# Kernel optimization log

Hardware: AMD Instinct MI355X
Metric: run time of the kernel (lower is better)

## Reference

```python
import jax, jax.numpy as jnp
import numpy as np

EPS = 1e-12  # matches torch F.normalize default eps
SCALE = 64.0  # fixed softmax temperature from the source

def _l2_normalize(x, axis):
    n = jnp.linalg.norm(x, ord=2, axis=axis, keepdims=True)
    return x / jnp.maximum(n, EPS)

def setup_inputs() -> dict:
    key = jax.random.key(0)
    k1, k2, k3 = jax.random.split(key, 3)
    B, L, S, D = 8, 2048, 2048, 128
    return {
        "query": jax.random.normal(k1, (B, L, D), dtype=jnp.float32),
        "key": jax.random.normal(k2, (B, S, D), dtype=jnp.float32),
        "value": jax.random.normal(k3, (B, S, D), dtype=jnp.float32),
    }

def reference(query, key, value):
    # rank-3 query path with norm=True, return_value=True, return_score=False
    q = _l2_normalize(query, axis=2)   # [B, L, D]
    k = _l2_normalize(key, axis=2)     # [B, S, D]
    score = jnp.einsum('nlk,nsk->nls', q, k)            # [B, L, S]
    score = jax.nn.softmax(score * SCALE, axis=2)
    # original does broadcast-multiply-then-sum; equivalent contraction:
    out = jnp.einsum('nls,nsd->nld', score, value)      # [B, L, D]
    return out
```

## Files before the change

### kernel.cpp

```cpp
#include <hip/hip_runtime.h>
#include <stdint.h>

#define Bb 8
#define Ll 2048
#define Ss 2048
#define Dd 128
#define NSB 8
#define SCHUNK 256
#define NROWS 16384
#define SCALE_LOG2E 92.33248261689366f

typedef __attribute__((ext_vector_type(8))) short bf16x8;
typedef __attribute__((ext_vector_type(16))) float f32x16;
typedef __attribute__((ext_vector_type(4))) unsigned u32x4;

__device__ __forceinline__ unsigned f2bf_pack(float a, float b) {
  unsigned ua = __float_as_uint(a); ua += 0x7fffu + ((ua >> 16) & 1u);
  unsigned ub = __float_as_uint(b); ub += 0x7fffu + ((ub >> 16) & 1u);
  return (ua >> 16) | (ub & 0xffff0000u);
}

__device__ __forceinline__ unsigned pkbf(float a, float b) {
#if __has_builtin(__builtin_amdgcn_cvt_pk_bf16_f32)
  auto r = __builtin_amdgcn_cvt_pk_bf16_f32(a, b);
  return __builtin_bit_cast(unsigned, r);
#else
  return f2bf_pack(a, b);
#endif
}

__device__ __forceinline__ void gl_lds16(const void* g, void* l) {
  __builtin_amdgcn_global_load_lds(
      (const __attribute__((address_space(1))) unsigned*)g,
      (__attribute__((address_space(3))) unsigned*)l, 16, 0, 0);
}


#define TRS 138
extern "C" __global__ __launch_bounds__(256)
void prep_kern(const float* __restrict__ Q, const float* __restrict__ K,
               const float* __restrict__ V,
               unsigned short* __restrict__ Qn, unsigned short* __restrict__ Kf,
               unsigned short* __restrict__ Vf) {
  __shared__ unsigned short T[32 * TRS];
  const int t = threadIdx.x;
  const int bid = blockIdx.x;
  if (bid < 8192) {
    const int lane = t & 63;
    int row = (bid << 2) + (t >> 6);
    const bool isK = row >= NROWS;
    const int r = isK ? row - NROWS : row;
    const float* src = isK ? K : Q;
    float2 f = *(const float2*)(src + (size_t)r * Dd + lane * 2);
    float ss = f.x * f.x + f.y * f.y;
#pragma unroll
    for (int m = 1; m < 64; m <<= 1) ss += __shfl_xor(ss, m, 64);
    float inv = 1.0f / fmaxf(sqrtf(ss), 1e-12f);
    unsigned w = pkbf(f.x * inv, f.y * inv);
    if (!isK) {
      *(unsigned*)(Qn + (size_t)r * Dd + lane * 2) = w;
    } else {
      const int srow = r & (Ss - 1);
      const int b = r >> 11;
      size_t off = (((size_t)b * 64 + (srow >> 5)) * 8 + (lane >> 3)) * 512 +
                   (((lane >> 2) & 1) * 32 + (srow & 31)) * 8 + ((2 * lane) & 7);
      *(unsigned*)(Kf + off) = w;
    }
  } else {
    const int vb = bid - 8192;
    const int b = vb & 7, sw = vb >> 3;
    const int d4 = t & 31, sr = t >> 5;
#pragma unroll
    for (int p = 0; p < 4; ++p) {
      int sl = p * 8 + sr;
      float4 v = *(const float4*)(V + ((size_t)(b * Ss + sw * 32 + sl)) * Dd + d4 * 4);
      *(unsigned*)&T[sl * TRS + d4 * 4]     = pkbf(v.x, v.y);
      *(unsigned*)&T[sl * TRS + d4 * 4 + 2] = pkbf(v.z, v.w);
    }
    __syncthreads();
    const int so = t & 3, db = t >> 2;
    const int t2 = so >> 1, h = so & 1;
#pragma unroll
    for (int p = 0; p < 2; ++p) {
      int d = p * 64 + db;
      unsigned u[4];
#pragma unroll
      for (int k = 0; k < 4; ++k) {
        unsigned lo = T[(so * 8 + 2 * k) * TRS + d];
        unsigned hi = T[(so * 8 + 2 * k + 1) * TRS + d];
        u[k] = lo | (hi << 16);
      }
      const int vslot = (d >> 5) * 2 + t2;
      size_t off = (((size_t)b * 64 + sw) * 8 + vslot) * 512 +
                   (h * 32 + (d & 31)) * 8;
      *(uint4*)(Vf + off) = make_uint4(u[0], u[1], u[2], u[3]);
    }
  }
}

extern "C" __global__ __launch_bounds__(256, 4)
void attn_kern(const unsigned short* __restrict__ Qn,
               const unsigned short* __restrict__ Kf,
               const unsigned short* __restrict__ Vf,
               unsigned short* __restrict__ Op,
               float* __restrict__ Lp) {
  __shared__ unsigned short Kl[2][8 * 512];
  __shared__ unsigned short Vl[2][8 * 512];
  const int tid = threadIdx.x, wv = tid >> 6, lane = tid & 63;
  const int lm = lane & 31, h = lane >> 5;
  const int gid = blockIdx.x;
  const int qt = gid >> 6, b = (gid >> 3) & 7, sb = gid & 7;
  const int sblk0 = sb * (SCHUNK / 32);
  const int qrow = qt * 128 + wv * 32 + lm;

  const unsigned short* Qrow = Qn + ((size_t)(b * Ll + qrow)) * Dd;
  bf16x8 qf[8];
#pragma unroll
  for (int kt = 0; kt < 8; ++kt)
    qf[kt] = *(const bf16x8*)(Qrow + kt * 16 + h * 8);

  const unsigned short* Kc = Kf + ((size_t)b * 64 + sblk0) * 8 * 512;
  const unsigned short* Vc = Vf + ((size_t)b * 64 + sblk0) * 8 * 512;

  f32x16 o[4];
#pragma unroll
  for (int i = 0; i < 4; ++i)
#pragma unroll
    for (int r = 0; r < 16; ++r) o[i][r] = 0.f;

  auto stage = [&](int it, int buf) {
    const size_t base = (size_t)it * 4096;
#pragma unroll
    for (int i = 0; i < 2; ++i) {
      const int sl = wv * 2 + i;
      gl_lds16(Kc + base + sl * 512 + lane * 8, &Kl[buf][sl * 512]);
      gl_lds16(Vc + base + sl * 512 + lane * 8, &Vl[buf][sl * 512]);
    }
  };
  stage(0, 0);

  float lrun = 0.f;

#pragma unroll 1
  for (int it = 0; it < 8; ++it) {
    __syncthreads();
    const int cur = it & 1;
    if (it + 1 < 8) stage(it + 1, cur ^ 1);

    f32x16 acc;
#pragma unroll
    for (int r = 0; r < 16; ++r) acc[r] = 0.f;
#pragma unroll
    for (int kt = 0; kt < 8; ++kt) {
      bf16x8 kf = *(const bf16x8*)&Kl[cur][kt * 512 + lane * 8];
      acc = __builtin_amdgcn_mfma_f32_32x32x16_bf16(kf, qf[kt], acc, 0, 0, 0);
    }

    float ls = 0.f;
#pragma unroll
    for (int t = 0; t < 2; ++t) {
      float p[8];
#pragma unroll
      for (int j = 0; j < 8; ++j)
        p[j] = __builtin_amdgcn_exp2f(
            __builtin_fmaf(acc[t * 8 + j], SCALE_LOG2E, -SCALE_LOG2E));
      ls += ((p[0] + p[1]) + (p[2] + p[3])) + ((p[4] + p[5]) + (p[6] + p[7]));
      unsigned u0 = pkbf(p[0], p[1]), u1 = pkbf(p[2], p[3]);
      unsigned u2 = pkbf(p[4], p[5]), u3 = pkbf(p[6], p[7]);
      unsigned s0p = (unsigned)__shfl_xor((int)u0, 32, 64);
      unsigned s1p = (unsigned)__shfl_xor((int)u1, 32, 64);
      unsigned s2p = (unsigned)__shfl_xor((int)u2, 32, 64);
      unsigned s3p = (unsigned)__shfl_xor((int)u3, 32, 64);
      u32x4 fr;
      fr.x = h ? s2p : u0;
      fr.y = h ? s3p : u1;
      fr.z = h ? u2 : s0p;
      fr.w = h ? u3 : s1p;
      bf16x8 pf = __builtin_bit_cast(bf16x8, fr);
#pragma unroll
      for (int dblk = 0; dblk < 4; ++dblk) {
        bf16x8 vf = *(const bf16x8*)&Vl[cur][(dblk * 2 + t) * 512 + lane * 8];
        o[dblk] = __builtin_amdgcn_mfma_f32_32x32x16_bf16(vf, pf, o[dblk], 0, 0, 0);
      }
    }
    lrun += ls;
  }

  const float lt = lrun + __shfl_xor(lrun, 32, 64);
  unsigned short* Ob = Op + ((size_t)sb * NROWS + b * Ll + qrow) * Dd;
#pragma unroll
  for (int dblk = 0; dblk < 4; ++dblk)
#pragma unroll
    for (int g = 0; g < 4; ++g) {
      uint2 w;
      w.x = pkbf(o[dblk][g * 4 + 0], o[dblk][g * 4 + 1]);
      w.y = pkbf(o[dblk][g * 4 + 2], o[dblk][g * 4 + 3]);
      *(uint2*)(Ob + dblk * 32 + g * 8 + h * 4) = w;
    }
  if (h == 0) Lp[sb * NROWS + b * Ll + qrow] = lt;
}

extern "C" __global__ __launch_bounds__(256)
void comb_kern(const unsigned short* __restrict__ Op,
               const float* __restrict__ Lp, float* __restrict__ Out) {
  const int idx = blockIdx.x * 256 + threadIdx.x;
  const int row = idx >> 5;
  const int dof = (idx & 31) * 4;
  float den = 0.f;
#pragma unroll
  for (int s = 0; s < NSB; ++s) den += Lp[s * NROWS + row];
  float a0 = 0.f, a1 = 0.f, a2 = 0.f, a3 = 0.f;
#pragma unroll
  for (int s = 0; s < NSB; ++s) {
    uint2 v = *(const uint2*)(Op + ((size_t)s * NROWS + row) * Dd + dof);
    a0 += __uint_as_float(v.x << 16);
    a1 += __uint_as_float(v.x & 0xffff0000u);
    a2 += __uint_as_float(v.y << 16);
    a3 += __uint_as_float(v.y & 0xffff0000u);
  }
  const float inv = 1.f / den;
  float4 r; r.x = a0 * inv; r.y = a1 * inv; r.z = a2 * inv; r.w = a3 * inv;
  *(float4*)(Out + (size_t)row * Dd + dof) = r;
}

extern "C" void kernel_launch(void* const* d_in, const int* in_sizes, int n_in,
                              void* d_out, int out_size, void* d_ws, size_t ws_size,
                              hipStream_t stream) {
  const float* Q = (const float*)d_in[0];
  const float* K = (const float*)d_in[1];
  const float* V = (const float*)d_in[2];
  float* Out = (float*)d_out;
  unsigned short* Qn = (unsigned short*)d_ws;
  unsigned short* Kf = Qn + (size_t)NROWS * Dd;
  unsigned short* Vf = Kf + (size_t)NROWS * Dd;
  unsigned short* Op = Vf + (size_t)Bb * Dd * Ss;
  float* Lp = (float*)(Op + (size_t)NSB * NROWS * Dd);
  hipLaunchKernelGGL(prep_kern, dim3(8192 + 512), dim3(256), 0, stream, Q, K, V, Qn, Kf, Vf);
  hipLaunchKernelGGL(attn_kern, dim3(1024), dim3(256), 0, stream, Qn, Kf, Vf, Op, Lp);
  hipLaunchKernelGGL(comb_kern, dim3(2048), dim3(256), 0, stream, Op, Lp, Out);
}
```

Measured before the change: 122.1 us.

## Load K/V fragments directly from global memory into registers, dropping LDS staging

Removes the double-buffered LDS staging of K and V tiles via global_load_lds and the per-iteration block barrier. Each wave now loads its K and V MFMA fragments straight from global memory into registers each iteration, relying on L2/cache for reuse across the four waves. Launch bounds are relaxed to 3 blocks per CU to make room for the extra fragment registers. This trades LDS traffic and sync for four times the global/L2 reads and no explicit prefetch overlap.

New measurement: 122.0 us. Within noise of the previous version (-0.1%).

```diff
diff --git a/kernel.cpp b/kernel.cpp
--- a/kernel.cpp
+++ b/kernel.cpp
@@ -27,12 +27,6 @@
 #else
   return f2bf_pack(a, b);
 #endif
-}
-
-__device__ __forceinline__ void gl_lds16(const void* g, void* l) {
-  __builtin_amdgcn_global_load_lds(
-      (const __attribute__((address_space(1))) unsigned*)g,
-      (__attribute__((address_space(3))) unsigned*)l, 16, 0, 0);
 }
 
 
@@ -98,14 +92,12 @@
   }
 }
 
-extern "C" __global__ __launch_bounds__(256, 4)
+extern "C" __global__ __launch_bounds__(256, 3)
 void attn_kern(const unsigned short* __restrict__ Qn,
                const unsigned short* __restrict__ Kf,
                const unsigned short* __restrict__ Vf,
                unsigned short* __restrict__ Op,
                float* __restrict__ Lp) {
-  __shared__ unsigned short Kl[2][8 * 512];
-  __shared__ unsigned short Vl[2][8 * 512];
   const int tid = threadIdx.x, wv = tid >> 6, lane = tid & 63;
   const int lm = lane & 31, h = lane >> 5;
   const int gid = blockIdx.x;
@@ -119,42 +111,37 @@
   for (int kt = 0; kt < 8; ++kt)
     qf[kt] = *(const bf16x8*)(Qrow + kt * 16 + h * 8);
 
-  const unsigned short* Kc = Kf + ((size_t)b * 64 + sblk0) * 8 * 512;
-  const unsigned short* Vc = Vf + ((size_t)b * 64 + sblk0) * 8 * 512;
+  const unsigned short* Kc = Kf + ((size_t)b * 64 + sblk0) * 8 * 512 + lane * 8;
+  const unsigned short* Vc = Vf + ((size_t)b * 64 + sblk0) * 8 * 512 + lane * 8;
 
   f32x16 o[4];
 #pragma unroll
   for (int i = 0; i < 4; ++i)
 #pragma unroll
     for (int r = 0; r < 16; ++r) o[i][r] = 0.f;
-
-  auto stage = [&](int it, int buf) {
-    const size_t base = (size_t)it * 4096;
-#pragma unroll
-    for (int i = 0; i < 2; ++i) {
-      const int sl = wv * 2 + i;
-      gl_lds16(Kc + base + sl * 512 + lane * 8, &Kl[buf][sl * 512]);
-      gl_lds16(Vc + base + sl * 512 + lane * 8, &Vl[buf][sl * 512]);
-    }
-  };
-  stage(0, 0);
 
   float lrun = 0.f;
 
 #pragma unroll 1
   for (int it = 0; it < 8; ++it) {
-    __syncthreads();
-    const int cur = it & 1;
-    if (it + 1 < 8) stage(it + 1, cur ^ 1);
+    const size_t base = (size_t)it * 4096;
+
+    bf16x8 kfr[8];
+#pragma unroll
+    for (int kt = 0; kt < 8; ++kt)
+      kfr[kt] = *(const bf16x8*)(Kc + base + kt * 512);
 
     f32x16 acc;
 #pragma unroll
     for (int r = 0; r < 16; ++r) acc[r] = 0.f;
 #pragma unroll
-    for (int kt = 0; kt < 8; ++kt) {
-      bf16x8 kf = *(const bf16x8*)&Kl[cur][kt * 512 + lane * 8];
-      acc = __builtin_amdgcn_mfma_f32_32x32x16_bf16(kf, qf[kt], acc, 0, 0, 0);
-    }
+    for (int kt = 0; kt < 8; ++kt)
+      acc = __builtin_amdgcn_mfma_f32_32x32x16_bf16(kfr[kt], qf[kt], acc, 0, 0, 0);
+
+    bf16x8 vfr[8];
+#pragma unroll
+    for (int vs = 0; vs < 8; ++vs)
+      vfr[vs] = *(const bf16x8*)(Vc + base + vs * 512);
 
     float ls = 0.f;
 #pragma unroll
@@ -178,10 +165,9 @@
       fr.w = h ? u3 : s1p;
       bf16x8 pf = __builtin_bit_cast(bf16x8, fr);
 #pragma unroll
-      for (int dblk = 0; dblk < 4; ++dblk) {
-        bf16x8 vf = *(const bf16x8*)&Vl[cur][(dblk * 2 + t) * 512 + lane * 8];
-        o[dblk] = __builtin_amdgcn_mfma_f32_32x32x16_bf16(vf, pf, o[dblk], 0, 0, 0);
-      }
+      for (int dblk = 0; dblk < 4; ++dblk)
+        o[dblk] = __builtin_amdgcn_mfma_f32_32x32x16_bf16(vfr[dblk * 2 + t], pf,
+                                                          o[dblk], 0, 0, 0);
     }
     lrun += ls;
   }
```
